# Kernel tuning notes

Hardware: AMD Instinct MI355X
Metric: run time of the kernel (lower is better)

The kernel has to match this reference:

```python
import jax, jax.numpy as jnp
import numpy as np

OW = 80                # cfg.out_size[1]
POS_THRESHOLD = 0.005  # cfg.pos_threshold
LN_EPS = 1e-5


def setup_inputs() -> dict:
    key = jax.random.key(0)
    ks = jax.random.split(key, 6)
    B, C, T, N = 16, 1024, 64, 12
    NFG = NFR = NFG_ONE = 1024
    s = 0.02
    return {
        "x": jax.random.normal(ks[0], (B, C, T, N), dtype=jnp.float32),
        "A": jax.random.uniform(ks[1], (B, T, N, 4), dtype=jnp.float32),
        "w_theta": jax.random.normal(ks[2], (NFG, NFR), dtype=jnp.float32) * s,
        "b_theta": jnp.zeros((NFR,), dtype=jnp.float32),
        "w_phi": jax.random.normal(ks[3], (NFG, NFR), dtype=jnp.float32) * s,
        "b_phi": jnp.zeros((NFR,), dtype=jnp.float32),
        "w_gcn": jax.random.normal(ks[4], (NFG, NFG_ONE), dtype=jnp.float32) * s,
        "ln_w": jnp.ones((N, NFG_ONE), dtype=jnp.float32),
        "ln_b": jnp.zeros((N, NFG_ONE), dtype=jnp.float32),
    }


def reference(x, A, w_theta, b_theta, w_phi, b_phi, w_gcn, ln_w, ln_b):
    B, C, T, N = x.shape
    # box centers -> pairwise euclidean distances per (B*T) frame
    boxes = A.reshape(-1, 4)
    cx = (boxes[:, 0] + boxes[:, 2]) * 0.5
    cy = (boxes[:, 1] + boxes[:, 3]) * 0.5
    pos = jnp.stack([cx, cy], axis=-1).reshape(B * T, N, 2)
    sq = jnp.sum(pos * pos, axis=2)  # [BT, N]
    d2 = sq[:, :, None] - 2.0 * jnp.einsum('bnc,bmc->bnm', pos, pos) + sq[:, None, :]
    dist = jnp.sqrt(jnp.maximum(d2, 0.0))  # clamp tiny negatives from fp error
    position_mask = dist > POS_THRESHOLD * OW  # [BT, N, N]

    # features: [B, C, T, N] -> [BT, N, C]
    feat = jnp.transpose(x, (0, 2, 3, 1)).reshape(B * T, N, C)
    theta = feat @ w_theta + b_theta  # [BT, N, NFR]
    phi = feat @ w_phi + b_phi        # [BT, N, NFR]
    scale = 1.0 / jnp.sqrt(jnp.asarray(theta.shape[-1], dtype=feat.dtype))
    logits = jnp.einsum('bnf,bmf->bnm', theta, phi) * scale
    logits = jnp.where(position_mask, -jnp.inf, logits)
    relation_graph = jax.nn.softmax(logits, axis=2)  # [BT, N, N]

    # graph conv: aggregate then project (no bias)
    agg = jnp.einsum('bnm,bmc->bnc', relation_graph, feat) @ w_gcn  # [BT, N, NFG_ONE]

    # LayerNorm over the last two dims [N, NFG_ONE]
    mu = jnp.mean(agg, axis=(1, 2), keepdims=True)
    var = jnp.var(agg, axis=(1, 2), keepdims=True)
    normed = (agg - mu) / jnp.sqrt(var + LN_EPS) * ln_w + ln_b
    out = jax.nn.relu(normed)
    return out, relation_graph
```

## Files before the change

kernel.cpp:

```cpp
#include <hip/hip_runtime.h>
#include <math.h>
#include <stdint.h>

#define NDIM   12
#define KDIM   1024
#define BT_TOT 1024
#define M_TOT  (BT_TOT * NDIM)
#define OUT_MAIN (M_TOT * KDIM)
#define MASK_TH 0.4f
#define LN_EPS 1e-5f

typedef float f32x4 __attribute__((ext_vector_type(4)));
typedef short bf16x8 __attribute__((ext_vector_type(8)));
typedef short bf16x4 __attribute__((ext_vector_type(4)));

__device__ __forceinline__ float bf2f(unsigned short u) {
    return __uint_as_float(((unsigned int)u) << 16);
}
__device__ __forceinline__ unsigned short f2bf(float f) {
    unsigned int u = __float_as_uint(f);
    return (unsigned short)((u + 0x7FFFu + ((u >> 16) & 1u)) >> 16);
}
__device__ __forceinline__ void gld16(const void* g, void* l) {
    __builtin_amdgcn_global_load_lds(
        (const __attribute__((address_space(1))) unsigned int*)g,
        (__attribute__((address_space(3))) unsigned int*)l, 16, 0, 0);
}

__global__ __launch_bounds__(256)
void castw_kernel(const float* __restrict__ wth, const float* __restrict__ wph,
                  unsigned short* __restrict__ t0, unsigned short* __restrict__ t1)
{
    const int bid = blockIdx.x;
    const float* src = bid < 512 ? wth : wph;
    unsigned short* dst = bid < 512 ? t0 : t1;
    const size_t off = (size_t)(bid & 511) * 2048 + (size_t)threadIdx.x * 8;
    const float4 a = *(const float4*)(src + off);
    const float4 b = *(const float4*)(src + off + 4);
    unsigned short o[8] = {f2bf(a.x), f2bf(a.y), f2bf(a.z), f2bf(a.w),
                           f2bf(b.x), f2bf(b.y), f2bf(b.z), f2bf(b.w)};
    *(uint4*)(dst + off) = *(const uint4*)o;
}

__global__ __launch_bounds__(256)
void transwg_kernel(const float* __restrict__ w, unsigned short* __restrict__ dst)
{
    __shared__ float tile[32][33];
    const int c0 = blockIdx.y * 32, o0 = blockIdx.x * 32;
    const int tx = threadIdx.x & 31, ty = threadIdx.x >> 5;
    #pragma unroll
    for (int i = 0; i < 4; ++i) {
        const int r = ty + i * 8;
        tile[r][tx] = w[(size_t)(c0 + r) * KDIM + o0 + tx];
    }
    __syncthreads();
    #pragma unroll
    for (int i = 0; i < 4; ++i) {
        const int r = ty + i * 8;
        dst[(size_t)(o0 + r) * KDIM + c0 + tx] = f2bf(tile[tx][r]);
    }
}

__global__ __launch_bounds__(256)
void featT_kernel(const float* __restrict__ x, unsigned short* __restrict__ featB)
{
    const int b = blockIdx.z;
    const int c0 = blockIdx.y * 32;
    const int p0 = blockIdx.x * 32;
    __shared__ float tile[32][33];
    const int tx = threadIdx.x & 31, ty = threadIdx.x >> 5;
    const float* src = x + (size_t)b * KDIM * 768;
    #pragma unroll
    for (int i = 0; i < 4; ++i) {
        const int cc = ty + i * 8;
        tile[cc][tx] = src[(size_t)(c0 + cc) * 768 + p0 + tx];
    }
    __syncthreads();
    unsigned short* dst = featB + (size_t)b * 768 * KDIM;
    #pragma unroll
    for (int i = 0; i < 4; ++i) {
        const int pp = ty + i * 8;
        dst[(size_t)(p0 + pp) * KDIM + c0 + tx] = f2bf(tile[tx][pp]);
    }
}

__global__ __launch_bounds__(256)
void biasv_kernel(const float* __restrict__ wph, const float* __restrict__ btheta,
                  float* __restrict__ v)
{
    const int lane = threadIdx.x & 63, w = threadIdx.x >> 6;
    const int j = blockIdx.x * 4 + w;
    const float4* row = (const float4*)(wph + (size_t)j * KDIM);
    const float4* bt4 = (const float4*)btheta;
    float s = 0.f;
    #pragma unroll
    for (int i = 0; i < 4; ++i) {
        const float4 a = row[lane + i * 64], b = bt4[lane + i * 64];
        s += a.x * b.x + a.y * b.y + a.z * b.z + a.w * b.w;
    }
    #pragma unroll
    for (int msk = 32; msk >= 1; msk >>= 1) s += __shfl_xor(s, msk, 64);
    if (lane == 0) v[j] = s;
}

__global__ __launch_bounds__(256)
void qk_kernel(const unsigned short* __restrict__ featB, const float* __restrict__ v,
               float* __restrict__ q)
{
    __shared__ float vS[KDIM];
    const int tid = threadIdx.x, lane = tid & 63, w = tid >> 6;
    #pragma unroll
    for (int i = 0; i < 4; ++i) vS[tid + i * 256] = v[tid + i * 256];
    __syncthreads();
    const int r = blockIdx.x * 4 + w;
    const unsigned short* row = featB + (size_t)r * KDIM;
    float s = 0.f;
    #pragma unroll
    for (int h = 0; h < 2; ++h) {
        const int e0 = h * 512 + lane * 8;
        const bf16x8 a = *(const bf16x8*)&row[e0];
        #pragma unroll
        for (int j = 0; j < 8; ++j)
            s = fmaf(bf2f((unsigned short)a[j]), vS[e0 + j], s);
    }
    #pragma unroll
    for (int msk = 32; msk >= 1; msk >>= 1) s += __shfl_xor(s, msk, 64);
    if (lane == 0) q[r] = s;
}

template<bool SWZ>
__global__ __launch_bounds__(256)
void gemm_kernel(const unsigned short* __restrict__ A,
                 const unsigned short* __restrict__ B0, const unsigned short* __restrict__ B1,
                 unsigned short* __restrict__ C0, unsigned short* __restrict__ C1)
{
    int m0, n0, zz;
    if (SWZ) {
        const int bid = blockIdx.x;
        const int c = bid & 7, s = bid >> 3;
        const int n = s & 7, mm = (s >> 3) % 12, z = s / 96;
        m0 = (c * 12 + mm) * 128; n0 = n * 128; zz = z;
    } else {
        m0 = blockIdx.y * 128; n0 = blockIdx.x * 128; zz = blockIdx.z;
    }
    const unsigned short* B = zz ? B1 : B0;
    unsigned short* C       = zz ? C1 : C0;

    const int tid = threadIdx.x, lane = tid & 63, wid = tid >> 6;
    const int wr = wid >> 1, wc = wid & 1;

    __shared__ __align__(16) unsigned short As[128 * 32];
    __shared__ __align__(16) unsigned short Bs[128 * 32];

    f32x4 acc[4][4] = {};

    const int srow = tid >> 2;
    const int scol = (tid & 3) * 16;

    for (int k0 = 0; k0 < KDIM; k0 += 32) {
        const char* gA = (const char*)A + ((size_t)(m0 + srow) * KDIM + k0) * 2 + scol;
        const char* gB = (const char*)B + ((size_t)(n0 + srow) * KDIM + k0) * 2 + scol;
        char* lA = (char*)As + wid * 1024;
        char* lB = (char*)Bs + wid * 1024;
        gld16(gA, lA);
        gld16(gA + (size_t)64 * KDIM * 2, lA + 4096);
        gld16(gB, lB);
        gld16(gB + (size_t)64 * KDIM * 2, lB + 4096);
        __syncthreads();

        bf16x8 af[4], bfr[4];
        const int rA = wr * 64 + (lane & 15);
        const int rB = wc * 64 + (lane & 15);
        const int kq = (lane >> 4) * 8;
        #pragma unroll
        for (int mi = 0; mi < 4; ++mi)
            af[mi] = *(const bf16x8*)&As[(rA + mi * 16) * 32 + kq];
        #pragma unroll
        for (int ni = 0; ni < 4; ++ni)
            bfr[ni] = *(const bf16x8*)&Bs[(rB + ni * 16) * 32 + kq];
        #pragma unroll
        for (int mi = 0; mi < 4; ++mi)
            #pragma unroll
            for (int ni = 0; ni < 4; ++ni)
                acc[mi][ni] = __builtin_amdgcn_mfma_f32_16x16x32_bf16(
                    af[mi], bfr[ni], acc[mi][ni], 0, 0, 0);
        __syncthreads();
    }

    #pragma unroll
    for (int mi = 0; mi < 4; ++mi) {
        const int gr0 = m0 + wr * 64 + mi * 16 + (lane >> 4) * 4;
        #pragma unroll
        for (int ni = 0; ni < 4; ++ni) {
            const int gc = n0 + wc * 64 + ni * 16 + (lane & 15);
            const f32x4 v = acc[mi][ni];
            #pragma unroll
            for (int reg = 0; reg < 4; ++reg)
                C[(size_t)(gr0 + reg) * KDIM + gc] = f2bf(v[reg]);
        }
    }
}

__global__ __launch_bounds__(256)
void relf_kernel(const unsigned short* __restrict__ G,
                 const unsigned short* __restrict__ featB,
                 const unsigned short* __restrict__ H,
                 const float* __restrict__ Abox, const float* __restrict__ q,
                 const float* __restrict__ lnw, const float* __restrict__ lnb,
                 float* __restrict__ out)
{
    const int f = blockIdx.x, tid = threadIdx.x, lane = tid & 63, w = tid >> 6;
    __shared__ float Lred[4][16][16];
    __shared__ float relS[12][12];
    __shared__ float cxS[12], cyS[12], sqS[12], qS[12];
    __shared__ float rs[2][256];

    if (tid < 12) {
        const float4 box = *(const float4*)(Abox + ((size_t)f * 12 + tid) * 4);
        const float cx = (box.x + box.z) * 0.5f, cy = (box.y + box.w) * 0.5f;
        cxS[tid] = cx; cyS[tid] = cy; sqS[tid] = cx * cx + cy * cy;
        qS[tid] = q[f * 12 + tid];
    }

    const int r = lane & 15, rr = r < 12 ? r : 0;
    const int kq = (lane >> 4) * 8;
    const unsigned short* gG = G + (size_t)(f * 12 + rr) * KDIM;
    const unsigned short* gF = featB + (size_t)(f * 12 + rr) * KDIM;
    f32x4 acc = {};
    #pragma unroll
    for (int s8 = 0; s8 < 8; ++s8) {
        const int k0 = (w * 8 + s8) * 32 + kq;
        const bf16x8 a = *(const bf16x8*)(gG + k0);
        const bf16x8 b = *(const bf16x8*)(gF + k0);
        acc = __builtin_amdgcn_mfma_f32_16x16x32_bf16(a, b, acc, 0, 0, 0);
    }
    {
        const int row0 = (lane >> 4) * 4, col = lane & 15;
        #pragma unroll
        for (int reg = 0; reg < 4; ++reg) Lred[w][row0 + reg][col] = acc[reg];
    }
    __syncthreads();

    if (tid < 12) {
        const int n = tid;
        float l[12], mx = -3.4e38f;
        #pragma unroll
        for (int m = 0; m < 12; ++m) {
            const float L = Lred[0][n][m] + Lred[1][n][m] + Lred[2][n][m] + Lred[3][n][m];
            float val = (L + qS[m]) * 0.03125f;
            const float d2 = sqS[n] - 2.f * (cxS[n] * cxS[m] + cyS[n] * cyS[m]) + sqS[m];
            const float dist = sqrtf(fmaxf(d2, 0.f));
            if (dist > MASK_TH) val = -INFINITY;
            l[m] = val; mx = fmaxf(mx, val);
        }
        float s = 0.f, e[12];
        #pragma unroll
        for (int m = 0; m < 12; ++m) { e[m] = expf(l[m] - mx); s += e[m]; }
        const float inv = 1.f / s;
        float* orel = out + (size_t)OUT_MAIN + (size_t)f * 144 + n * 12;
        #pragma unroll
        for (int m = 0; m < 12; ++m) {
            const float rv = e[m] * inv;
            relS[n][m] = rv;
            orel[m] = rv;
        }
    }
    __syncthreads();

    const int c0 = tid * 4;
    float h[12][4];
    #pragma unroll
    for (int m = 0; m < 12; ++m) {
        const bf16x4 h4 = *(const bf16x4*)(H + (size_t)(f * 12 + m) * KDIM + c0);
        #pragma unroll
        for (int j = 0; j < 4; ++j) h[m][j] = bf2f((unsigned short)h4[j]);
    }
    float a2[12][4];
    float s = 0.f, s2 = 0.f;
    #pragma unroll
    for (int n = 0; n < 12; ++n) {
        float rn[12];
        #pragma unroll
        for (int m = 0; m < 12; ++m) rn[m] = relS[n][m];
        #pragma unroll
        for (int j = 0; j < 4; ++j) {
            float a = 0.f;
            #pragma unroll
            for (int m = 0; m < 12; ++m) a = fmaf(rn[m], h[m][j], a);
            a2[n][j] = a; s += a; s2 += a * a;
        }
    }
    rs[0][tid] = s; rs[1][tid] = s2;
    __syncthreads();
    for (int o = 128; o > 0; o >>= 1) {
        if (tid < o) { rs[0][tid] += rs[0][tid + o]; rs[1][tid] += rs[1][tid + o]; }
        __syncthreads();
    }
    const float mu = rs[0][0] * (1.f / 12288.f);
    const float var = rs[1][0] * (1.f / 12288.f) - mu * mu;
    const float rstd = rsqrtf(var + LN_EPS);

    #pragma unroll
    for (int n = 0; n < 12; ++n) {
        const float4 wv = *(const float4*)(lnw + (size_t)n * KDIM + c0);
        const float4 bv = *(const float4*)(lnb + (size_t)n * KDIM + c0);
        float4 ov;
        ov.x = fmaxf(fmaf((a2[n][0] - mu) * rstd, wv.x, bv.x), 0.f);
        ov.y = fmaxf(fmaf((a2[n][1] - mu) * rstd, wv.y, bv.y), 0.f);
        ov.z = fmaxf(fmaf((a2[n][2] - mu) * rstd, wv.z, bv.z), 0.f);
        ov.w = fmaxf(fmaf((a2[n][3] - mu) * rstd, wv.w, bv.w), 0.f);
        *(float4*)(out + (size_t)(f * 12 + n) * KDIM + c0) = ov;
    }
}

extern "C" void kernel_launch(void* const* d_in, const int* in_sizes, int n_in,
                              void* d_out, int out_size, void* d_ws, size_t ws_size,
                              hipStream_t stream) {
    const float* x   = (const float*)d_in[0];
    const float* A   = (const float*)d_in[1];
    const float* wth = (const float*)d_in[2];
    const float* bth = (const float*)d_in[3];
    const float* wph = (const float*)d_in[4];
    const float* wg  = (const float*)d_in[6];
    const float* lnw = (const float*)d_in[7];
    const float* lnb = (const float*)d_in[8];
    float* out = (float*)d_out;

    char* ws = (char*)d_ws;
    const size_t MB = 1ull << 20;
    unsigned short* featB = (unsigned short*)(ws);
    unsigned short* G     = (unsigned short*)(ws + 24 * MB);
    unsigned short* H     = (unsigned short*)(ws + 48 * MB);
    unsigned short* wth_b = (unsigned short*)(ws + 72 * MB);
    unsigned short* wph_b = (unsigned short*)(ws + 74 * MB);
    unsigned short* wgT   = (unsigned short*)(ws + 76 * MB);
    unsigned short* MtB   = (unsigned short*)(ws + 78 * MB);
    float* vbuf = (float*)(ws + 80 * MB);
    float* qbuf = (float*)(ws + 80 * MB + 4096);

    castw_kernel<<<1024, 256, 0, stream>>>(wth, wph, wth_b, wph_b);
    transwg_kernel<<<dim3(32, 32), 256, 0, stream>>>(wg, wgT);
    featT_kernel<<<dim3(24, 32, 16), 256, 0, stream>>>(x, featB);
    biasv_kernel<<<256, 256, 0, stream>>>(wph, bth, vbuf);
    qk_kernel<<<3072, 256, 0, stream>>>(featB, vbuf, qbuf);
    gemm_kernel<false><<<dim3(8, 8, 1), 256, 0, stream>>>(
        wph_b, wth_b, wth_b, MtB, MtB);
    gemm_kernel<true><<<1536, 256, 0, stream>>>(
        featB, MtB, wgT, G, H);
    relf_kernel<<<BT_TOT, 256, 0, stream>>>(G, featB, H, A, qbuf, lnw, lnb, out);
}
```

Before: 234.6 us.

## Fuse prep kernels, fold qk into relf, widen GEMM K-tile with swizzled LDS

Merges the cast, transpose, feature-transpose and bias-vector kernels into one prep launch. The per-row q dot product moves into the relation kernel, which reads featB rows it already touches and removes a separate pass and launch. The GEMM K step grows from 32 to 64 and uses an XOR-swizzled LDS layout, halving the barrier count and cutting bank conflicts. The cost is more LDS per block and some added work inside relf.

Result: faster. 220.6 us (-6.0%).

```diff
diff --git a/kernel.cpp b/kernel.cpp
--- a/kernel.cpp
+++ b/kernel.cpp
@@ -28,104 +28,76 @@
 }
 
 __global__ __launch_bounds__(256)
-void castw_kernel(const float* __restrict__ wth, const float* __restrict__ wph,
-                  unsigned short* __restrict__ t0, unsigned short* __restrict__ t1)
+void prep_kernel(const float* __restrict__ x,   const float* __restrict__ wth,
+                 const float* __restrict__ wph, const float* __restrict__ bth,
+                 const float* __restrict__ wg,
+                 unsigned short* __restrict__ wth_b, unsigned short* __restrict__ wph_b,
+                 unsigned short* __restrict__ wgT,   float* __restrict__ vbuf,
+                 unsigned short* __restrict__ featB)
 {
-    const int bid = blockIdx.x;
-    const float* src = bid < 512 ? wth : wph;
-    unsigned short* dst = bid < 512 ? t0 : t1;
-    const size_t off = (size_t)(bid & 511) * 2048 + (size_t)threadIdx.x * 8;
-    const float4 a = *(const float4*)(src + off);
-    const float4 b = *(const float4*)(src + off + 4);
-    unsigned short o[8] = {f2bf(a.x), f2bf(a.y), f2bf(a.z), f2bf(a.w),
-                           f2bf(b.x), f2bf(b.y), f2bf(b.z), f2bf(b.w)};
-    *(uint4*)(dst + off) = *(const uint4*)o;
-}
-
-__global__ __launch_bounds__(256)
-void transwg_kernel(const float* __restrict__ w, unsigned short* __restrict__ dst)
-{
-    __shared__ float tile[32][33];
-    const int c0 = blockIdx.y * 32, o0 = blockIdx.x * 32;
-    const int tx = threadIdx.x & 31, ty = threadIdx.x >> 5;
-    #pragma unroll
-    for (int i = 0; i < 4; ++i) {
-        const int r = ty + i * 8;
-        tile[r][tx] = w[(size_t)(c0 + r) * KDIM + o0 + tx];
-    }
-    __syncthreads();
-    #pragma unroll
-    for (int i = 0; i < 4; ++i) {
-        const int r = ty + i * 8;
-        dst[(size_t)(o0 + r) * KDIM + c0 + tx] = f2bf(tile[tx][r]);
-    }
-}
-
-__global__ __launch_bounds__(256)
-void featT_kernel(const float* __restrict__ x, unsigned short* __restrict__ featB)
-{
-    const int b = blockIdx.z;
-    const int c0 = blockIdx.y * 32;
-    const int p0 = blockIdx.x * 32;
-    __shared__ float tile[32][33];
-    const int tx = threadIdx.x & 31, ty = threadIdx.x >> 5;
-    const float* src = x + (size_t)b * KDIM * 768;
-    #pragma unroll
-    for (int i = 0; i < 4; ++i) {
-        const int cc = ty + i * 8;
-        tile[cc][tx] = src[(size_t)(c0 + cc) * 768 + p0 + tx];
-    }
-    __syncthreads();
-    unsigned short* dst = featB + (size_t)b * 768 * KDIM;
-    #pragma unroll
-    for (int i = 0; i < 4; ++i) {
-        const int pp = ty + i * 8;
-        dst[(size_t)(p0 + pp) * KDIM + c0 + tx] = f2bf(tile[tx][pp]);
-    }
-}
-
-__global__ __launch_bounds__(256)
-void biasv_kernel(const float* __restrict__ wph, const float* __restrict__ btheta,
-                  float* __restrict__ v)
-{
-    const int lane = threadIdx.x & 63, w = threadIdx.x >> 6;
-    const int j = blockIdx.x * 4 + w;
-    const float4* row = (const float4*)(wph + (size_t)j * KDIM);
-    const float4* bt4 = (const float4*)btheta;
-    float s = 0.f;
-    #pragma unroll
-    for (int i = 0; i < 4; ++i) {
-        const float4 a = row[lane + i * 64], b = bt4[lane + i * 64];
-        s += a.x * b.x + a.y * b.y + a.z * b.z + a.w * b.w;
-    }
-    #pragma unroll
-    for (int msk = 32; msk >= 1; msk >>= 1) s += __shfl_xor(s, msk, 64);
-    if (lane == 0) v[j] = s;
-}
-
-__global__ __launch_bounds__(256)
-void qk_kernel(const unsigned short* __restrict__ featB, const float* __restrict__ v,
-               float* __restrict__ q)
-{
-    __shared__ float vS[KDIM];
-    const int tid = threadIdx.x, lane = tid & 63, w = tid >> 6;
-    #pragma unroll
-    for (int i = 0; i < 4; ++i) vS[tid + i * 256] = v[tid + i * 256];
-    __syncthreads();
-    const int r = blockIdx.x * 4 + w;
-    const unsigned short* row = featB + (size_t)r * KDIM;
-    float s = 0.f;
-    #pragma unroll
-    for (int h = 0; h < 2; ++h) {
-        const int e0 = h * 512 + lane * 8;
-        const bf16x8 a = *(const bf16x8*)&row[e0];
-        #pragma unroll
-        for (int j = 0; j < 8; ++j)
-            s = fmaf(bf2f((unsigned short)a[j]), vS[e0 + j], s);
-    }
-    #pragma unroll
-    for (int msk = 32; msk >= 1; msk >>= 1) s += __shfl_xor(s, msk, 64);
-    if (lane == 0) q[r] = s;
+    const int bid = blockIdx.x, tid = threadIdx.x;
+    __shared__ float tileF[64][33];
+
+    if (bid < 1024) {
+        const float* src = bid < 512 ? wth : wph;
+        unsigned short* dst = bid < 512 ? wth_b : wph_b;
+        const size_t off = (size_t)(bid & 511) * 2048 + (size_t)tid * 8;
+        const float4 a = *(const float4*)(src + off);
+        const float4 b = *(const float4*)(src + off + 4);
+        unsigned short o[8] = {f2bf(a.x), f2bf(a.y), f2bf(a.z), f2bf(a.w),
+                               f2bf(b.x), f2bf(b.y), f2bf(b.z), f2bf(b.w)};
+        *(uint4*)(dst + off) = *(const uint4*)o;
+    } else if (bid < 2048) {
+        const int b2 = bid - 1024;
+        const int o0 = (b2 & 31) * 32, c0 = (b2 >> 5) * 32;
+        const int tx = tid & 31, ty = tid >> 5;
+        #pragma unroll
+        for (int i = 0; i < 4; ++i) {
+            const int r = ty + i * 8;
+            tileF[r][tx] = wg[(size_t)(c0 + r) * KDIM + o0 + tx];
+        }
+        __syncthreads();
+        #pragma unroll
+        for (int i = 0; i < 4; ++i) {
+            const int r = ty + i * 8;
+            wgT[(size_t)(o0 + r) * KDIM + c0 + tx] = f2bf(tileF[tx][r]);
+        }
+    } else if (bid < 2304) {
+        const int b3 = bid - 2048;
+        const int lane = tid & 63, w = tid >> 6;
+        const int j = b3 * 4 + w;
+        const float4* row = (const float4*)(wph + (size_t)j * KDIM);
+        const float4* bt4 = (const float4*)bth;
+        float s = 0.f;
+        #pragma unroll
+        for (int i = 0; i < 4; ++i) {
+            const float4 a = row[lane + i * 64], b = bt4[lane + i * 64];
+            s += a.x * b.x + a.y * b.y + a.z * b.z + a.w * b.w;
+        }
+        #pragma unroll
+        for (int msk = 32; msk >= 1; msk >>= 1) s += __shfl_xor(s, msk, 64);
+        if (lane == 0) vbuf[j] = s;
+    } else {
+        const int b4 = bid - 2304;
+        const int px = b4 % 24;
+        const int rest = b4 / 24;
+        const int cx = rest & 15, b = rest >> 4;
+        const int p0 = px * 32, c0 = cx * 64;
+        const float* src = x + (size_t)b * KDIM * 768;
+        #pragma unroll
+        for (int i = 0; i < 8; ++i) {
+            const int cl = (tid >> 5) + i * 8;
+            tileF[cl][tid & 31] = src[(size_t)(c0 + cl) * 768 + p0 + (tid & 31)];
+        }
+        __syncthreads();
+        unsigned short* dst = featB + ((size_t)b * 768 + p0) * KDIM;
+        #pragma unroll
+        for (int i = 0; i < 8; ++i) {
+            const int pp = (tid >> 6) + i * 4;
+            const int cl = tid & 63;
+            dst[(size_t)pp * KDIM + c0 + cl] = f2bf(tileF[cl][pp]);
+        }
+    }
 }
 
 template<bool SWZ>
@@ -149,41 +121,49 @@
     const int tid = threadIdx.x, lane = tid & 63, wid = tid >> 6;
     const int wr = wid >> 1, wc = wid & 1;
 
-    __shared__ __align__(16) unsigned short As[128 * 32];
-    __shared__ __align__(16) unsigned short Bs[128 * 32];
+    __shared__ __align__(16) unsigned short As[128 * 64];
+    __shared__ __align__(16) unsigned short Bs[128 * 64];
 
     f32x4 acc[4][4] = {};
 
-    const int srow = tid >> 2;
-    const int scol = (tid & 3) * 16;
-
-    for (int k0 = 0; k0 < KDIM; k0 += 32) {
-        const char* gA = (const char*)A + ((size_t)(m0 + srow) * KDIM + k0) * 2 + scol;
-        const char* gB = (const char*)B + ((size_t)(n0 + srow) * KDIM + k0) * 2 + scol;
-        char* lA = (char*)As + wid * 1024;
-        char* lB = (char*)Bs + wid * 1024;
-        gld16(gA, lA);
-        gld16(gA + (size_t)64 * KDIM * 2, lA + 4096);
-        gld16(gB, lB);
-        gld16(gB + (size_t)64 * KDIM * 2, lB + 4096);
-        __syncthreads();
-
-        bf16x8 af[4], bfr[4];
-        const int rA = wr * 64 + (lane & 15);
-        const int rB = wc * 64 + (lane & 15);
-        const int kq = (lane >> 4) * 8;
-        #pragma unroll
-        for (int mi = 0; mi < 4; ++mi)
-            af[mi] = *(const bf16x8*)&As[(rA + mi * 16) * 32 + kq];
-        #pragma unroll
-        for (int ni = 0; ni < 4; ++ni)
-            bfr[ni] = *(const bf16x8*)&Bs[(rB + ni * 16) * 32 + kq];
-        #pragma unroll
-        for (int mi = 0; mi < 4; ++mi)
-            #pragma unroll
-            for (int ni = 0; ni < 4; ++ni)
-                acc[mi][ni] = __builtin_amdgcn_mfma_f32_16x16x32_bf16(
-                    af[mi], bfr[ni], acc[mi][ni], 0, 0, 0);
+    const int srow_w = wid * 8 + (lane >> 3);
+    const int schunk = lane & 7;
+
+    for (int k0 = 0; k0 < KDIM; k0 += 64) {
+        #pragma unroll
+        for (int i = 0; i < 4; ++i) {
+            const int row = srow_w + i * 32;
+            const int gchunk = schunk ^ (row & 7);
+            const char* srcA = (const char*)A + ((size_t)(m0 + row) * KDIM + k0) * 2 + gchunk * 16;
+            const char* srcB = (const char*)B + ((size_t)(n0 + row) * KDIM + k0) * 2 + gchunk * 16;
+            char* la = (char*)As + i * 4096 + wid * 1024;
+            char* lb = (char*)Bs + i * 4096 + wid * 1024;
+            gld16(srcA, la);
+            gld16(srcB, lb);
+        }
+        __syncthreads();
+
+        #pragma unroll
+        for (int ks = 0; ks < 2; ++ks) {
+            bf16x8 af[4], bfr[4];
+            const int cch = ks * 4 + (lane >> 4);
+            #pragma unroll
+            for (int mi = 0; mi < 4; ++mi) {
+                const int r = wr * 64 + (lane & 15) + mi * 16;
+                af[mi] = *(const bf16x8*)((const char*)As + r * 128 + ((cch ^ (r & 7)) * 16));
+            }
+            #pragma unroll
+            for (int ni = 0; ni < 4; ++ni) {
+                const int r = wc * 64 + (lane & 15) + ni * 16;
+                bfr[ni] = *(const bf16x8*)((const char*)Bs + r * 128 + ((cch ^ (r & 7)) * 16));
+            }
+            #pragma unroll
+            for (int mi = 0; mi < 4; ++mi)
+                #pragma unroll
+                for (int ni = 0; ni < 4; ++ni)
+                    acc[mi][ni] = __builtin_amdgcn_mfma_f32_16x16x32_bf16(
+                        af[mi], bfr[ni], acc[mi][ni], 0, 0, 0);
+        }
         __syncthreads();
     }
 
@@ -205,21 +185,21 @@
 void relf_kernel(const unsigned short* __restrict__ G,
                  const unsigned short* __restrict__ featB,
                  const unsigned short* __restrict__ H,
-                 const float* __restrict__ Abox, const float* __restrict__ q,
+                 const float* __restrict__ Abox, const float* __restrict__ vbuf,
                  const float* __restrict__ lnw, const float* __restrict__ lnb,
                  float* __restrict__ out)
 {
     const int f = blockIdx.x, tid = threadIdx.x, lane = tid & 63, w = tid >> 6;
     __shared__ float Lred[4][16][16];
     __shared__ float relS[12][12];
-    __shared__ float cxS[12], cyS[12], sqS[12], qS[12];
+    __shared__ float cxS[12], cyS[12], sqS[12];
+    __shared__ float qred[4][12];
     __shared__ float rs[2][256];
 
     if (tid < 12) {
         const float4 box = *(const float4*)(Abox + ((size_t)f * 12 + tid) * 4);
         const float cx = (box.x + box.z) * 0.5f, cy = (box.y + box.w) * 0.5f;
         cxS[tid] = cx; cyS[tid] = cy; sqS[tid] = cx * cx + cy * cy;
-        qS[tid] = q[f * 12 + tid];
     }
 
     const int r = lane & 15, rr = r < 12 ? r : 0;
@@ -239,6 +219,26 @@
         #pragma unroll
         for (int reg = 0; reg < 4; ++reg) Lred[w][row0 + reg][col] = acc[reg];
     }
+
+    const int c0 = tid * 4;
+    {
+        const float4 v4 = *(const float4*)(vbuf + c0);
+        float qp[12];
+        #pragma unroll
+        for (int m = 0; m < 12; ++m) {
+            const bf16x4 fm = *(const bf16x4*)(featB + (size_t)(f * 12 + m) * KDIM + c0);
+            qp[m] = bf2f((unsigned short)fm[0]) * v4.x + bf2f((unsigned short)fm[1]) * v4.y
+                  + bf2f((unsigned short)fm[2]) * v4.z + bf2f((unsigned short)fm[3]) * v4.w;
+        }
+        #pragma unroll
+        for (int msk = 32; msk >= 1; msk >>= 1)
+            #pragma unroll
+            for (int m = 0; m < 12; ++m) qp[m] += __shfl_xor(qp[m], msk, 64);
+        if (lane == 0) {
+            #pragma unroll
+            for (int m = 0; m < 12; ++m) qred[w][m] = qp[m];
+        }
+    }
     __syncthreads();
 
     if (tid < 12) {
@@ -247,7 +247,8 @@
         #pragma unroll
         for (int m = 0; m < 12; ++m) {
             const float L = Lred[0][n][m] + Lred[1][n][m] + Lred[2][n][m] + Lred[3][n][m];
-            float val = (L + qS[m]) * 0.03125f;
+            const float qm = qred[0][m] + qred[1][m] + qred[2][m] + qred[3][m];
+            float val = (L + qm) * 0.03125f;
             const float d2 = sqS[n] - 2.f * (cxS[n] * cxS[m] + cyS[n] * cyS[m]) + sqS[m];
             const float dist = sqrtf(fmaxf(d2, 0.f));
             if (dist > MASK_TH) val = -INFINITY;
@@ -267,7 +268,6 @@
     }
     __syncthreads();
 
-    const int c0 = tid * 4;
     float h[12][4];
     #pragma unroll
     for (int m = 0; m < 12; ++m) {
@@ -336,16 +336,12 @@
     unsigned short* wgT   = (unsigned short*)(ws + 76 * MB);
     unsigned short* MtB   = (unsigned short*)(ws + 78 * MB);
     float* vbuf = (float*)(ws + 80 * MB);
-    float* qbuf = (float*)(ws + 80 * MB + 4096);
-
-    castw_kernel<<<1024, 256, 0, stream>>>(wth, wph, wth_b, wph_b);
-    transwg_kernel<<<dim3(32, 32), 256, 0, stream>>>(wg, wgT);
-    featT_kernel<<<dim3(24, 32, 16), 256, 0, stream>>>(x, featB);
-    biasv_kernel<<<256, 256, 0, stream>>>(wph, bth, vbuf);
-    qk_kernel<<<3072, 256, 0, stream>>>(featB, vbuf, qbuf);
+
+    prep_kernel<<<8448, 256, 0, stream>>>(x, wth, wph, bth, wg,
+                                          wth_b, wph_b, wgT, vbuf, featB);
     gemm_kernel<false><<<dim3(8, 8, 1), 256, 0, stream>>>(
         wph_b, wth_b, wth_b, MtB, MtB);
     gemm_kernel<true><<<1536, 256, 0, stream>>>(
         featB, MtB, wgT, G, H);
-    relf_kernel<<<BT_TOT, 256, 0, stream>>>(G, featB, H, A, qbuf, lnw, lnb, out);
-}
+    relf_kernel<<<BT_TOT, 256, 0, stream>>>(G, featB, H, A, vbuf, lnw, lnb, out);
+}
```
